# Kernel optimization log

Measured on AMD Instinct MI355X. Metric: run time of the kernel, lower is better.

The kernel has to match this reference:

```python
import jax, jax.numpy as jnp
import numpy as np
from jax import lax

INPUT_DIM = 4
HIDDEN_DIM = 32
PRED_STEPS = 50
BATCH = 32768
SEQ_LEN = 200


def setup_inputs() -> dict:
    key = jax.random.key(0)
    ks = jax.random.split(key, 7)
    s = 1.0 / np.sqrt(HIDDEN_DIM)  # PyTorch LSTM init scale
    return {
        "history_data": jax.random.normal(ks[0], (BATCH, SEQ_LEN, INPUT_DIM), dtype=jnp.float32),
        "W_ih": jax.random.uniform(ks[1], (4 * HIDDEN_DIM, INPUT_DIM), jnp.float32, -s, s),
        "W_hh": jax.random.uniform(ks[2], (4 * HIDDEN_DIM, HIDDEN_DIM), jnp.float32, -s, s),
        "b_ih": jax.random.uniform(ks[3], (4 * HIDDEN_DIM,), jnp.float32, -s, s),
        "b_hh": jax.random.uniform(ks[4], (4 * HIDDEN_DIM,), jnp.float32, -s, s),
        "W_pred": jax.random.uniform(ks[5], (INPUT_DIM, HIDDEN_DIM), jnp.float32, -s, s),
        "b_pred": jax.random.uniform(ks[6], (INPUT_DIM,), jnp.float32, -s, s),
    }


def reference(history_data, W_ih, W_hh, b_ih, b_hh, W_pred, b_pred):
    H = W_hh.shape[1]
    b = b_ih + b_hh

    def cell(h, c, x):
        # PyTorch gate order: input, forget, cell(g), output
        gates = x @ W_ih.T + h @ W_hh.T + b  # [B, 4H]
        i, f, g, o = jnp.split(gates, 4, axis=-1)
        c_new = jax.nn.sigmoid(f) * c + jax.nn.sigmoid(i) * jnp.tanh(g)
        h_new = jax.nn.sigmoid(o) * jnp.tanh(c_new)
        return h_new, c_new

    B = history_data.shape[0]
    h0 = jnp.zeros((B, H), history_data.dtype)
    c0 = jnp.zeros((B, H), history_data.dtype)

    # Encode history: scan over time
    xs = jnp.swapaxes(history_data, 0, 1)  # [T, B, D]

    def hist_step(carry, x):
        h, c = carry
        h, c = cell(h, c, x)
        return (h, c), None

    (h, _), _ = lax.scan(hist_step, (h0, c0), xs)

    # each step (torch.zeros_like), carrying only h.
    def dec_step(h, _):
        pred = h @ W_pred.T + b_pred  # [B, INPUT_DIM]
        h_new, _ = cell(h, jnp.zeros_like(h), pred)
        return h_new, pred

    _, preds = lax.scan(dec_step, h, None, length=PRED_STEPS)  # [P, B, D]
    return jnp.swapaxes(preds, 0, 1)  # [B, PRED_STEPS, D]
```

## Files before the change

kernel.cpp:

```cpp
#include <hip/hip_runtime.h>
#include <math.h>

#define BATCH 32768
#define SEQLEN 200
#define PSTEPS 50
#define HID 32
#define LDS_PAD 36

typedef __attribute__((ext_vector_type(2))) _Float16 half2v;
typedef __attribute__((ext_vector_type(8))) _Float16 half8v;
typedef __attribute__((ext_vector_type(2))) __fp16   fp16x2;
typedef __attribute__((ext_vector_type(4))) float floatx4;

#define EXP2 __builtin_amdgcn_exp2f
#define RCPF __builtin_amdgcn_rcpf
#define PKRTZ __builtin_amdgcn_cvt_pkrtz
#define MED3 __builtin_amdgcn_fmed3f

#define L1C 1.4426950408889634f
#define L2C 2.8853900817779268f

union H8 { unsigned int u[4]; half8v h; half2v h2[4]; };
union HU { fp16x2 h; unsigned int u; };

__device__ __forceinline__ unsigned int pk(float a, float b) {
    HU t; t.h = PKRTZ(a, b); return t.u;
}

__global__ __launch_bounds__(256, 2)
void lstm_mfma_kernel(const float* __restrict__ hist, const float* __restrict__ W_ih,
                      const float* __restrict__ W_hh, const float* __restrict__ b_ih,
                      const float* __restrict__ b_hh, const float* __restrict__ W_pred,
                      const float* __restrict__ b_pred, float* __restrict__ out)
{
    const int lane = threadIdx.x & 63;
    const int wv   = threadIdx.x >> 6;
    const int m    = lane & 15;
    const int quad = lane >> 4;
    const int elem0 = (blockIdx.x * 4 + wv) * 16;

    if ((blockIdx.x >> 8) & 1) __builtin_amdgcn_s_sleep(12);

    __shared__ __align__(16) float h_lds_all[4][16][LDS_PAD];
    float (*hl)[LDS_PAD] = h_lds_all[wv];

    const float esc[4] = { -L1C, -L1C, L2C, -L1C };
    half8v Bh[8], B2[8];
    #pragma unroll
    for (int n = 0; n < 8; ++n) {
        const int gc = n * 16 + m;
        const float sc = esc[n >> 1];
        H8 bh;
        #pragma unroll
        for (int jj = 0; jj < 4; ++jj) {
            bh.h2[jj] = (half2v){ (_Float16)(sc * W_hh[gc * HID + quad * 8 + 2 * jj]),
                                  (_Float16)(sc * W_hh[gc * HID + quad * 8 + 2 * jj + 1]) };
        }
        Bh[n] = bh.h;
        H8 b2; b2.u[0] = b2.u[1] = b2.u[2] = b2.u[3] = 0u;
        if (quad == 0) {
            b2.h2[0] = (half2v){ (_Float16)(sc * W_ih[gc * 4 + 0]), (_Float16)(sc * W_ih[gc * 4 + 1]) };
            b2.h2[1] = (half2v){ (_Float16)(sc * W_ih[gc * 4 + 2]), (_Float16)(sc * W_ih[gc * 4 + 3]) };
            float bsum = sc * (b_ih[gc] + b_hh[gc]);
            _Float16 bhi = (_Float16)bsum;
            _Float16 blo = (_Float16)(bsum - (float)bhi);
            b2.h2[2] = (half2v){ bhi, blo };
        }
        B2[n] = b2.h;
    }
    const unsigned int one2 = 0x3C003C00u;

    float cst[2][4];
    #pragma unroll
    for (int hf = 0; hf < 2; ++hf)
        #pragma unroll
        for (int r = 0; r < 4; ++r) { cst[hf][r] = 0.f; hl[quad * 4 + r][hf * 16 + m] = 0.f; }
    asm volatile("s_waitcnt lgkmcnt(0)" ::: "memory");

    const float4* xp = (const float4*)(hist + (size_t)(elem0 + m) * (SEQLEN * 4));
    float4 xv = xp[0];
    #pragma unroll 1
    for (int t = 0; t < SEQLEN; ++t) {
        float4 h0 = *(const float4*)&hl[m][quad * 8];
        float4 h1 = *(const float4*)&hl[m][quad * 8 + 4];
        H8 ahu;
        ahu.u[0] = pk(h0.x, h0.y); ahu.u[1] = pk(h0.z, h0.w);
        ahu.u[2] = pk(h1.x, h1.y); ahu.u[3] = pk(h1.z, h1.w);
        const half8v ah = ahu.h;

        const unsigned int tx0 = pk(xv.x, xv.y), tx1 = pk(xv.z, xv.w);
        H8 a2u;
        a2u.u[0] = (quad == 0) ? tx0 : 0u;
        a2u.u[1] = (quad == 0) ? tx1 : 0u;
        a2u.u[2] = (quad == 0) ? one2 : 0u;
        a2u.u[3] = 0u;
        const half8v a2 = a2u.h;

        const int tn = (t + 1 < SEQLEN) ? t + 1 : SEQLEN - 1;
        float4 xn = xp[tn];

        floatx4 acc[8];
        #pragma unroll
        for (int n = 0; n < 8; ++n) {
            floatx4 a = __builtin_amdgcn_mfma_f32_16x16x32_f16(a2, B2[n], (floatx4){0.f,0.f,0.f,0.f}, 0, 0, 0);
            acc[n] = __builtin_amdgcn_mfma_f32_16x16x32_f16(ah, Bh[n], a, 0, 0, 0);
        }
        #pragma unroll
        for (int hf = 0; hf < 2; ++hf) {
            #pragma unroll
            for (int pr = 0; pr < 2; ++pr) {
                const int r0 = pr * 2, r1 = r0 + 1;
                const float eiA = EXP2(acc[0 + hf][r0]), eiB = EXP2(acc[0 + hf][r1]);
                const float efA = EXP2(acc[2 + hf][r0]), efB = EXP2(acc[2 + hf][r1]);
                const float egA = EXP2(acc[4 + hf][r0]), egB = EXP2(acc[4 + hf][r1]);
                const float eoA = EXP2(acc[6 + hf][r0]), eoB = EXP2(acc[6 + hf][r1]);
                const float pfA = 1.f + efA,                  pfB = 1.f + efB;
                const float t1A = (1.f + eiA) * (1.f + egA),  t1B = (1.f + eiB) * (1.f + egB);
                const float numA = fmaf(cst[hf][r0], t1A, (egA - 1.f) * pfA);
                const float numB = fmaf(cst[hf][r1], t1B, (egB - 1.f) * pfB);
                const float dA = t1A * pfA, dB = t1B * pfB;
                const float R  = RCPF(dA * dB);
                const float cnA = numA * (R * dB);
                const float cnB = numB * (R * dA);
                const float ecA = EXP2(MED3(cnA, -12.f, 12.f) * L2C);
                const float ecB = EXP2(MED3(cnB, -12.f, 12.f) * L2C);
                const float dhA = (1.f + eoA) * (1.f + ecA);
                const float dhB = (1.f + eoB) * (1.f + ecB);
                const float Rh  = RCPF(dhA * dhB);
                const float hnA = (ecA - 1.f) * (Rh * dhB);
                const float hnB = (ecB - 1.f) * (Rh * dhA);

                cst[hf][r0] = cnA; cst[hf][r1] = cnB;
                hl[quad * 4 + r0][hf * 16 + m] = hnA;
                hl[quad * 4 + r1][hf * 16 + m] = hnB;
            }
        }
        asm volatile("s_waitcnt lgkmcnt(0)" ::: "memory");
        xv = xn;
    }

    float wp[4][8];
    #pragma unroll
    for (int d = 0; d < 4; ++d)
        #pragma unroll
        for (int j = 0; j < 8; ++j) wp[d][j] = W_pred[d * HID + quad * 8 + j];
    float bp[4] = { b_pred[0], b_pred[1], b_pred[2], b_pred[3] };

    float* op = out + (size_t)(elem0 + m) * (PSTEPS * 4);
    #pragma unroll 1
    for (int p = 0; p < PSTEPS; ++p) {
        float4 h0 = *(const float4*)&hl[m][quad * 8];
        float4 h1 = *(const float4*)&hl[m][quad * 8 + 4];
        const float hv[8] = { h0.x, h0.y, h0.z, h0.w, h1.x, h1.y, h1.z, h1.w };

        float pd[4];
        #pragma unroll
        for (int d = 0; d < 4; ++d) {
            float s = 0.f;
            #pragma unroll
            for (int j = 0; j < 8; ++j) s = fmaf(hv[j], wp[d][j], s);
            s += __shfl_xor(s, 16);
            s += __shfl_xor(s, 32);
            pd[d] = s + bp[d];
        }
        if (quad == 0) *(float4*)(op + p * 4) = make_float4(pd[0], pd[1], pd[2], pd[3]);

        if (p + 1 < PSTEPS) {
            H8 ahu;
            ahu.u[0] = pk(hv[0], hv[1]); ahu.u[1] = pk(hv[2], hv[3]);
            ahu.u[2] = pk(hv[4], hv[5]); ahu.u[3] = pk(hv[6], hv[7]);
            const half8v ah = ahu.h;
            const unsigned int tx0 = pk(pd[0], pd[1]), tx1 = pk(pd[2], pd[3]);
            H8 a2u;
            a2u.u[0] = (quad == 0) ? tx0 : 0u;
            a2u.u[1] = (quad == 0) ? tx1 : 0u;
            a2u.u[2] = (quad == 0) ? one2 : 0u;
            a2u.u[3] = 0u;
            const half8v a2 = a2u.h;

            floatx4 acc[6];
            #pragma unroll
            for (int nn = 0; nn < 6; ++nn) {
                const int n = (nn < 2) ? nn : nn + 2;
                floatx4 a = __builtin_amdgcn_mfma_f32_16x16x32_f16(a2, B2[n], (floatx4){0.f,0.f,0.f,0.f}, 0, 0, 0);
                acc[nn] = __builtin_amdgcn_mfma_f32_16x16x32_f16(ah, Bh[n], a, 0, 0, 0);
            }
            #pragma unroll
            for (int hf = 0; hf < 2; ++hf) {
                #pragma unroll
                for (int pr = 0; pr < 2; ++pr) {
                    const int r0 = pr * 2, r1 = r0 + 1;
                    const float eiA = EXP2(acc[0 + hf][r0]), eiB = EXP2(acc[0 + hf][r1]);
                    const float egA = EXP2(acc[2 + hf][r0]), egB = EXP2(acc[2 + hf][r1]);
                    const float eoA = EXP2(acc[4 + hf][r0]), eoB = EXP2(acc[4 + hf][r1]);
                    const float dA = (1.f + eiA) * (1.f + egA);
                    const float dB = (1.f + eiB) * (1.f + egB);
                    const float R  = RCPF(dA * dB);
                    const float cnA = (egA - 1.f) * (R * dB);
                    const float cnB = (egB - 1.f) * (R * dA);
                    const float ecA = EXP2(cnA * L2C);
                    const float ecB = EXP2(cnB * L2C);
                    const float dhA = (1.f + eoA) * (1.f + ecA);
                    const float dhB = (1.f + eoB) * (1.f + ecB);
                    const float Rh  = RCPF(dhA * dhB);
                    const float hnA = (ecA - 1.f) * (Rh * dhB);
                    const float hnB = (ecB - 1.f) * (Rh * dhA);

                    hl[quad * 4 + r0][hf * 16 + m] = hnA;
                    hl[quad * 4 + r1][hf * 16 + m] = hnB;
                }
            }
            asm volatile("s_waitcnt lgkmcnt(0)" ::: "memory");
        }
    }
}

extern "C" void kernel_launch(void* const* d_in, const int* in_sizes, int n_in,
                              void* d_out, int out_size, void* d_ws, size_t ws_size,
                              hipStream_t stream) {
    const float* hist   = (const float*)d_in[0];
    const float* W_ih   = (const float*)d_in[1];
    const float* W_hh   = (const float*)d_in[2];
    const float* b_ih   = (const float*)d_in[3];
    const float* b_hh   = (const float*)d_in[4];
    const float* W_pred = (const float*)d_in[5];
    const float* b_pred = (const float*)d_in[6];
    float* out = (float*)d_out;

    const int blocks = (BATCH / 16) / 4;
    lstm_mfma_kernel<<<blocks, 256, 0, stream>>>(hist, W_ih, W_hh, b_ih, b_hh,
                                                 W_pred, b_pred, out);
}
```

Before: 399.7 us.

## Interleave two independent 16-row batch tiles per wavefront for ILP

Each wavefront now processes two independent 16-element batch tiles (A and B), issuing both sets of MFMAs before the gate math so that the two recurrence chains can hide each other's MFMA and transcendental latency. The grid is halved to 256 blocks, launch bounds drop to one block per SIMD group, and the staggered s_sleep for odd block groups is removed. Register pressure roughly doubles, and fewer waves are resident per CU, so latency hiding moves from wave-level to instruction-level parallelism.

Result: slower. 459.0 us (+14.9%).

```diff
diff --git a/kernel.cpp b/kernel.cpp
--- a/kernel.cpp
+++ b/kernel.cpp
@@ -27,7 +27,7 @@
     HU t; t.h = PKRTZ(a, b); return t.u;
 }
 
-__global__ __launch_bounds__(256, 2)
+__global__ __launch_bounds__(256, 1)
 void lstm_mfma_kernel(const float* __restrict__ hist, const float* __restrict__ W_ih,
                       const float* __restrict__ W_hh, const float* __restrict__ b_ih,
                       const float* __restrict__ b_hh, const float* __restrict__ W_pred,
@@ -37,12 +37,13 @@
     const int wv   = threadIdx.x >> 6;
     const int m    = lane & 15;
     const int quad = lane >> 4;
-    const int elem0 = (blockIdx.x * 4 + wv) * 16;
-
-    if ((blockIdx.x >> 8) & 1) __builtin_amdgcn_s_sleep(12);
-
-    __shared__ __align__(16) float h_lds_all[4][16][LDS_PAD];
-    float (*hl)[LDS_PAD] = h_lds_all[wv];
+    const int gidx  = blockIdx.x * 4 + wv;
+    const int elemA = gidx * 32;
+    const int elemB = elemA + 16;
+
+    __shared__ __align__(16) float h_lds_all[4][2][16][LDS_PAD];
+    float (*hlA)[LDS_PAD] = h_lds_all[wv][0];
+    float (*hlB)[LDS_PAD] = h_lds_all[wv][1];
 
     const float esc[4] = { -L1C, -L1C, L2C, -L1C };
     half8v Bh[8], B2[8];
@@ -70,54 +71,80 @@
     }
     const unsigned int one2 = 0x3C003C00u;
 
-    float cst[2][4];
+    float cstA[2][4], cstB[2][4];
     #pragma unroll
     for (int hf = 0; hf < 2; ++hf)
         #pragma unroll
-        for (int r = 0; r < 4; ++r) { cst[hf][r] = 0.f; hl[quad * 4 + r][hf * 16 + m] = 0.f; }
+        for (int r = 0; r < 4; ++r) {
+            cstA[hf][r] = 0.f; cstB[hf][r] = 0.f;
+            hlA[quad * 4 + r][hf * 16 + m] = 0.f;
+            hlB[quad * 4 + r][hf * 16 + m] = 0.f;
+        }
     asm volatile("s_waitcnt lgkmcnt(0)" ::: "memory");
 
-    const float4* xp = (const float4*)(hist + (size_t)(elem0 + m) * (SEQLEN * 4));
-    float4 xv = xp[0];
+    const float4* xpA = (const float4*)(hist + (size_t)(elemA + m) * (SEQLEN * 4));
+    const float4* xpB = (const float4*)(hist + (size_t)(elemB + m) * (SEQLEN * 4));
+    float4 xvA = xpA[0];
+    float4 xvB = xpB[0];
     #pragma unroll 1
     for (int t = 0; t < SEQLEN; ++t) {
-        float4 h0 = *(const float4*)&hl[m][quad * 8];
-        float4 h1 = *(const float4*)&hl[m][quad * 8 + 4];
-        H8 ahu;
-        ahu.u[0] = pk(h0.x, h0.y); ahu.u[1] = pk(h0.z, h0.w);
-        ahu.u[2] = pk(h1.x, h1.y); ahu.u[3] = pk(h1.z, h1.w);
-        const half8v ah = ahu.h;
-
-        const unsigned int tx0 = pk(xv.x, xv.y), tx1 = pk(xv.z, xv.w);
-        H8 a2u;
-        a2u.u[0] = (quad == 0) ? tx0 : 0u;
-        a2u.u[1] = (quad == 0) ? tx1 : 0u;
-        a2u.u[2] = (quad == 0) ? one2 : 0u;
-        a2u.u[3] = 0u;
-        const half8v a2 = a2u.h;
+        float4 hA0 = *(const float4*)&hlA[m][quad * 8];
+        float4 hA1 = *(const float4*)&hlA[m][quad * 8 + 4];
+        H8 ahuA;
+        ahuA.u[0] = pk(hA0.x, hA0.y); ahuA.u[1] = pk(hA0.z, hA0.w);
+        ahuA.u[2] = pk(hA1.x, hA1.y); ahuA.u[3] = pk(hA1.z, hA1.w);
+        const half8v ahA = ahuA.h;
+        const unsigned int txA0 = pk(xvA.x, xvA.y), txA1 = pk(xvA.z, xvA.w);
+        H8 a2uA;
+        a2uA.u[0] = (quad == 0) ? txA0 : 0u;
+        a2uA.u[1] = (quad == 0) ? txA1 : 0u;
+        a2uA.u[2] = (quad == 0) ? one2 : 0u;
+        a2uA.u[3] = 0u;
+        const half8v a2A = a2uA.h;
+
+        float4 hB0 = *(const float4*)&hlB[m][quad * 8];
+        float4 hB1 = *(const float4*)&hlB[m][quad * 8 + 4];
+        H8 ahuB;
+        ahuB.u[0] = pk(hB0.x, hB0.y); ahuB.u[1] = pk(hB0.z, hB0.w);
+        ahuB.u[2] = pk(hB1.x, hB1.y); ahuB.u[3] = pk(hB1.z, hB1.w);
+        const half8v ahB = ahuB.h;
+        const unsigned int txB0 = pk(xvB.x, xvB.y), txB1 = pk(xvB.z, xvB.w);
+        H8 a2uB;
+        a2uB.u[0] = (quad == 0) ? txB0 : 0u;
+        a2uB.u[1] = (quad == 0) ? txB1 : 0u;
+        a2uB.u[2] = (quad == 0) ? one2 : 0u;
+        a2uB.u[3] = 0u;
+        const half8v a2B = a2uB.h;
 
         const int tn = (t + 1 < SEQLEN) ? t + 1 : SEQLEN - 1;
-        float4 xn = xp[tn];
-
-        floatx4 acc[8];
+        float4 xnA = xpA[tn];
+        float4 xnB = xpB[tn];
+
+        floatx4 accA[8], accB[8];
         #pragma unroll
         for (int n = 0; n < 8; ++n) {
-            floatx4 a = __builtin_amdgcn_mfma_f32_16x16x32_f16(a2, B2[n], (floatx4){0.f,0.f,0.f,0.f}, 0, 0, 0);
-            acc[n] = __builtin_amdgcn_mfma_f32_16x16x32_f16(ah, Bh[n], a, 0, 0, 0);
-        }
+            floatx4 a = __builtin_amdgcn_mfma_f32_16x16x32_f16(a2A, B2[n], (floatx4){0.f,0.f,0.f,0.f}, 0, 0, 0);
+            accA[n] = __builtin_amdgcn_mfma_f32_16x16x32_f16(ahA, Bh[n], a, 0, 0, 0);
+        }
+        #pragma unroll
+        for (int n = 0; n < 8; ++n) {
+            floatx4 a = __builtin_amdgcn_mfma_f32_16x16x32_f16(a2B, B2[n], (floatx4){0.f,0.f,0.f,0.f}, 0, 0, 0);
+            accB[n] = __builtin_amdgcn_mfma_f32_16x16x32_f16(ahB, Bh[n], a, 0, 0, 0);
+        }
+
         #pragma unroll
         for (int hf = 0; hf < 2; ++hf) {
             #pragma unroll
             for (int pr = 0; pr < 2; ++pr) {
                 const int r0 = pr * 2, r1 = r0 + 1;
-                const float eiA = EXP2(acc[0 + hf][r0]), eiB = EXP2(acc[0 + hf][r1]);
-                const float efA = EXP2(acc[2 + hf][r0]), efB = EXP2(acc[2 + hf][r1]);
-                const float egA = EXP2(acc[4 + hf][r0]), egB = EXP2(acc[4 + hf][r1]);
-                const float eoA = EXP2(acc[6 + hf][r0]), eoB = EXP2(acc[6 + hf][r1]);
+                const float eiA = EXP2(accA[0 + hf][r0]), eiB = EXP2(accA[0 + hf][r1]);
+                const float efA = EXP2(accA[2 + hf][r0]), efB = EXP2(accA[2 + hf][r1]);
+                const float egA = EXP2(accA[4 + hf][r0]), egB = EXP2(accA[4 + hf][r1]);
+                const float eoA = EXP2(accA[6 + hf][r0]), eoB = EXP2(accA[6 + hf][r1]);
                 const float pfA = 1.f + efA,                  pfB = 1.f + efB;
                 const float t1A = (1.f + eiA) * (1.f + egA),  t1B = (1.f + eiB) * (1.f + egB);
-                const float numA = fmaf(cst[hf][r0], t1A, (egA - 1.f) * pfA);
-                const float numB = fmaf(cst[hf][r1], t1B, (egB - 1.f) * pfB);
+                const float numA = fmaf(cstA[hf][r0], t1A, (egA - 1.f) * pfA);
+                const float numB = fmaf(cstA[hf][r1], t1B, (egB - 1.f) * pfB);
                 const float dA = t1A * pfA, dB = t1B * pfB;
                 const float R  = RCPF(dA * dB);
                 const float cnA = numA * (R * dB);
@@ -130,13 +157,43 @@
                 const float hnA = (ecA - 1.f) * (Rh * dhB);
                 const float hnB = (ecB - 1.f) * (Rh * dhA);
 
-                cst[hf][r0] = cnA; cst[hf][r1] = cnB;
-                hl[quad * 4 + r0][hf * 16 + m] = hnA;
-                hl[quad * 4 + r1][hf * 16 + m] = hnB;
+                cstA[hf][r0] = cnA; cstA[hf][r1] = cnB;
+                hlA[quad * 4 + r0][hf * 16 + m] = hnA;
+                hlA[quad * 4 + r1][hf * 16 + m] = hnB;
+            }
+        }
+        #pragma unroll
+        for (int hf = 0; hf < 2; ++hf) {
+            #pragma unroll
+            for (int pr = 0; pr < 2; ++pr) {
+                const int r0 = pr * 2, r1 = r0 + 1;
+                const float eiA = EXP2(accB[0 + hf][r0]), eiB = EXP2(accB[0 + hf][r1]);
+                const float efA = EXP2(accB[2 + hf][r0]), efB = EXP2(accB[2 + hf][r1]);
+                const float egA = EXP2(accB[4 + hf][r0]), egB = EXP2(accB[4 + hf][r1]);
+                const float eoA = EXP2(accB[6 + hf][r0]), eoB = EXP2(accB[6 + hf][r1]);
+                const float pfA = 1.f + efA,                  pfB = 1.f + efB;
+                const float t1A = (1.f + eiA) * (1.f + egA),  t1B = (1.f + eiB) * (1.f + egB);
+                const float numA = fmaf(cstB[hf][r0], t1A, (egA - 1.f) * pfA);
+                const float numB = fmaf(cstB[hf][r1], t1B, (egB - 1.f) * pfB);
+                const float dA = t1A * pfA, dB = t1B * pfB;
+                const float R  = RCPF(dA * dB);
+                const float cnA = numA * (R * dB);
+                const float cnB = numB * (R * dA);
+                const float ecA = EXP2(MED3(cnA, -12.f, 12.f) * L2C);
+                const float ecB = EXP2(MED3(cnB, -12.f, 12.f) * L2C);
+                const float dhA = (1.f + eoA) * (1.f + ecA);
+                const float dhB = (1.f + eoB) * (1.f + ecB);
+                const float Rh  = RCPF(dhA * dhB);
+                const float hnA = (ecA - 1.f) * (Rh * dhB);
+                const float hnB = (ecB - 1.f) * (Rh * dhA);
+
+                cstB[hf][r0] = cnA; cstB[hf][r1] = cnB;
+                hlB[quad * 4 + r0][hf * 16 + m] = hnA;
+                hlB[quad * 4 + r1][hf * 16 + m] = hnB;
             }
         }
         asm volatile("s_waitcnt lgkmcnt(0)" ::: "memory");
-        xv = xn;
+        xvA = xnA; xvB = xnB;
     }
 
     float wp[4][8];
@@ -146,53 +203,80 @@
         for (int j = 0; j < 8; ++j) wp[d][j] = W_pred[d * HID + quad * 8 + j];
     float bp[4] = { b_pred[0], b_pred[1], b_pred[2], b_pred[3] };
 
-    float* op = out + (size_t)(elem0 + m) * (PSTEPS * 4);
+    float* opA = out + (size_t)(elemA + m) * (PSTEPS * 4);
+    float* opB = out + (size_t)(elemB + m) * (PSTEPS * 4);
     #pragma unroll 1
-    for (int p = 0; p < PSTEPS; ++p) {
-        float4 h0 = *(const float4*)&hl[m][quad * 8];
-        float4 h1 = *(const float4*)&hl[m][quad * 8 + 4];
-        const float hv[8] = { h0.x, h0.y, h0.z, h0.w, h1.x, h1.y, h1.z, h1.w };
-
-        float pd[4];
+    for (int ps = 0; ps < PSTEPS; ++ps) {
+        float4 hA0 = *(const float4*)&hlA[m][quad * 8];
+        float4 hA1 = *(const float4*)&hlA[m][quad * 8 + 4];
+        const float hvA[8] = { hA0.x, hA0.y, hA0.z, hA0.w, hA1.x, hA1.y, hA1.z, hA1.w };
+        float4 hB0 = *(const float4*)&hlB[m][quad * 8];
+        float4 hB1 = *(const float4*)&hlB[m][quad * 8 + 4];
+        const float hvB[8] = { hB0.x, hB0.y, hB0.z, hB0.w, hB1.x, hB1.y, hB1.z, hB1.w };
+
+        float pdA[4], pdB[4];
         #pragma unroll
         for (int d = 0; d < 4; ++d) {
-            float s = 0.f;
-            #pragma unroll
-            for (int j = 0; j < 8; ++j) s = fmaf(hv[j], wp[d][j], s);
-            s += __shfl_xor(s, 16);
-            s += __shfl_xor(s, 32);
-            pd[d] = s + bp[d];
-        }
-        if (quad == 0) *(float4*)(op + p * 4) = make_float4(pd[0], pd[1], pd[2], pd[3]);
-
-        if (p + 1 < PSTEPS) {
-            H8 ahu;
-            ahu.u[0] = pk(hv[0], hv[1]); ahu.u[1] = pk(hv[2], hv[3]);
-            ahu.u[2] = pk(hv[4], hv[5]); ahu.u[3] = pk(hv[6], hv[7]);
-            const half8v ah = ahu.h;
-            const unsigned int tx0 = pk(pd[0], pd[1]), tx1 = pk(pd[2], pd[3]);
-            H8 a2u;
-            a2u.u[0] = (quad == 0) ? tx0 : 0u;
-            a2u.u[1] = (quad == 0) ? tx1 : 0u;
-            a2u.u[2] = (quad == 0) ? one2 : 0u;
-            a2u.u[3] = 0u;
-            const half8v a2 = a2u.h;
-
-            floatx4 acc[6];
+            float sA = 0.f, sB = 0.f;
+            #pragma unroll
+            for (int j = 0; j < 8; ++j) { sA = fmaf(hvA[j], wp[d][j], sA); sB = fmaf(hvB[j], wp[d][j], sB); }
+            sA += __shfl_xor(sA, 16); sA += __shfl_xor(sA, 32);
+            sB += __shfl_xor(sB, 16); sB += __shfl_xor(sB, 32);
+            pdA[d] = sA + bp[d];
+            pdB[d] = sB + bp[d];
+        }
+        if (quad == 0) {
+            *(float4*)(opA + ps * 4) = make_float4(pdA[0], pdA[1], pdA[2], pdA[3]);
+            *(float4*)(opB + ps * 4) = make_float4(pdB[0], pdB[1], pdB[2], pdB[3]);
+        }
+
+        if (ps + 1 < PSTEPS) {
+            H8 ahuA;
+            ahuA.u[0] = pk(hvA[0], hvA[1]); ahuA.u[1] = pk(hvA[2], hvA[3]);
+            ahuA.u[2] = pk(hvA[4], hvA[5]); ahuA.u[3] = pk(hvA[6], hvA[7]);
+            const half8v ahA = ahuA.h;
+            const unsigned int txA0 = pk(pdA[0], pdA[1]), txA1 = pk(pdA[2], pdA[3]);
+            H8 a2uA;
+            a2uA.u[0] = (quad == 0) ? txA0 : 0u;
+            a2uA.u[1] = (quad == 0) ? txA1 : 0u;
+            a2uA.u[2] = (quad == 0) ? one2 : 0u;
+            a2uA.u[3] = 0u;
+            const half8v a2A = a2uA.h;
+
+            H8 ahuB;
+            ahuB.u[0] = pk(hvB[0], hvB[1]); ahuB.u[1] = pk(hvB[2], hvB[3]);
+            ahuB.u[2] = pk(hvB[4], hvB[5]); ahuB.u[3] = pk(hvB[6], hvB[7]);
+            const half8v ahB = ahuB.h;
+            const unsigned int txB0 = pk(pdB[0], pdB[1]), txB1 = pk(pdB[2], pdB[3]);
+            H8 a2uB;
+            a2uB.u[0] = (quad == 0) ? txB0 : 0u;
+            a2uB.u[1] = (quad == 0) ? txB1 : 0u;
+            a2uB.u[2] = (quad == 0) ? one2 : 0u;
+            a2uB.u[3] = 0u;
+            const half8v a2B = a2uB.h;
+
+            floatx4 accA[6], accB[6];
             #pragma unroll
             for (int nn = 0; nn < 6; ++nn) {
                 const int n = (nn < 2) ? nn : nn + 2;
-                floatx4 a = __builtin_amdgcn_mfma_f32_16x16x32_f16(a2, B2[n], (floatx4){0.f,0.f,0.f,0.f}, 0, 0, 0);
-                acc[nn] = __builtin_amdgcn_mfma_f32_16x16x32_f16(ah, Bh[n], a, 0, 0, 0);
-            }
+                floatx4 a = __builtin_amdgcn_mfma_f32_16x16x32_f16(a2A, B2[n], (floatx4){0.f,0.f,0.f,0.f}, 0, 0, 0);
+                accA[nn] = __builtin_amdgcn_mfma_f32_16x16x32_f16(ahA, Bh[n], a, 0, 0, 0);
+            }
+            #pragma unroll
+            for (int nn = 0; nn < 6; ++nn) {
+                const int n = (nn < 2) ? nn : nn + 2;
+                floatx4 a = __builtin_amdgcn_mfma_f32_16x16x32_f16(a2B, B2[n], (floatx4){0.f,0.f,0.f,0.f}, 0, 0, 0);
+                accB[nn] = __builtin_amdgcn_mfma_f32_16x16x32_f16(ahB, Bh[n], a, 0, 0, 0);
+            }
+
             #pragma unroll
             for (int hf = 0; hf < 2; ++hf) {
                 #pragma unroll
                 for (int pr = 0; pr < 2; ++pr) {
                     const int r0 = pr * 2, r1 = r0 + 1;
-                    const float eiA = EXP2(acc[0 + hf][r0]), eiB = EXP2(acc[0 + hf][r1]);
-                    const float egA = EXP2(acc[2 + hf][r0]), egB = EXP2(acc[2 + hf][r1]);
-                    const float eoA = EXP2(acc[4 + hf][r0]), eoB = EXP2(acc[4 + hf][r1]);
+                    const float eiA = EXP2(accA[0 + hf][r0]), eiB = EXP2(accA[0 + hf][r1]);
+                    const float egA = EXP2(accA[2 + hf][r0]), egB = EXP2(accA[2 + hf][r1]);
+                    const float eoA = EXP2(accA[4 + hf][r0]), eoB = EXP2(accA[4 + hf][r1]);
                     const float dA = (1.f + eiA) * (1.f + egA);
                     const float dB = (1.f + eiB) * (1.f + egB);
                     const float R  = RCPF(dA * dB);
@@ -206,8 +290,33 @@
                     const float hnA = (ecA - 1.f) * (Rh * dhB);
                     const float hnB = (ecB - 1.f) * (Rh * dhA);
 
-                    hl[quad * 4 + r0][hf * 16 + m] = hnA;
-                    hl[quad * 4 + r1][hf * 16 + m] = hnB;
+                    hlA[quad * 4 + r0][hf * 16 + m] = hnA;
+                    hlA[quad * 4 + r1][hf * 16 + m] = hnB;
+                }
+            }
+            #pragma unroll
+            for (int hf = 0; hf < 2; ++hf) {
+                #pragma unroll
+                for (int pr = 0; pr < 2; ++pr) {
+                    const int r0 = pr * 2, r1 = r0 + 1;
+                    const float eiA = EXP2(accB[0 + hf][r0]), eiB = EXP2(accB[0 + hf][r1]);
+                    const float egA = EXP2(accB[2 + hf][r0]), egB = EXP2(accB[2 + hf][r1]);
+                    const float eoA = EXP2(accB[4 + hf][r0]), eoB = EXP2(accB[4 + hf][r1]);
+                    const float dA = (1.f + eiA) * (1.f + egA);
+                    const float dB = (1.f + eiB) * (1.f + egB);
+                    const float R  = RCPF(dA * dB);
+                    const float cnA = (egA - 1.f) * (R * dB);
+                    const float cnB = (egB - 1.f) * (R * dA);
+                    const float ecA = EXP2(cnA * L2C);
+                    const float ecB = EXP2(cnB * L2C);
+                    const float dhA = (1.f + eoA) * (1.f + ecA);
+                    const float dhB = (1.f + eoB) * (1.f + ecB);
+                    const float Rh  = RCPF(dhA * dhB);
+                    const float hnA = (ecA - 1.f) * (Rh * dhB);
+                    const float hnB = (ecB - 1.f) * (Rh * dhA);
+
+                    hlB[quad * 4 + r0][hf * 16 + m] = hnA;
+                    hlB[quad * 4 + r1][hf * 16 + m] = hnB;
                 }
             }
             asm volatile("s_waitcnt lgkmcnt(0)" ::: "memory");
@@ -227,7 +336,7 @@
     const float* b_pred = (const float*)d_in[6];
     float* out = (float*)d_out;
 
-    const int blocks = (BATCH / 16) / 4;
+    const int blocks = BATCH / 128;
     lstm_mfma_kernel<<<blocks, 256, 0, stream>>>(hist, W_ih, W_hh, b_ih, b_hh,
                                                  W_pred, b_pred, out);
 }
```
